# Performance work log

Measured on AMD Instinct MI355X. Metric: run time of the kernel, lower is better.

The kernel has to match this reference:

```python
import jax, jax.numpy as jnp
import numpy as np

N_NODES = 100000
N_EDGES = 1600000
IN_CH, HID_CH, OUT_CH = 128, 128, 64


def _spmm(row, col, val, x, n):
    # COO sparse @ dense: out[r] += val_e * x[col_e]
    gathered = val[:, None] * x[col]  # [E, d]
    return jax.ops.segment_sum(gathered, row, num_segments=n)


def setup_inputs() -> dict:
    key = jax.random.key(0)
    ks = jax.random.split(key, 8)
    x = jax.random.normal(ks[0], (N_NODES, IN_CH), dtype=jnp.float32)
    adj_row = jax.random.randint(ks[1], (N_EDGES,), 0, N_NODES)
    adj_col = jax.random.randint(ks[2], (N_EDGES,), 0, N_NODES)
    adj_val = jax.random.uniform(ks[3], (N_EDGES,), dtype=jnp.float32)
    w1 = jax.random.normal(ks[4], (IN_CH, HID_CH), dtype=jnp.float32) * (1.0 / np.sqrt(IN_CH))
    b1 = jax.random.normal(ks[5], (HID_CH,), dtype=jnp.float32) * 0.01
    w2 = jax.random.normal(ks[6], (HID_CH, OUT_CH), dtype=jnp.float32) * (1.0 / np.sqrt(HID_CH))
    b2 = jax.random.normal(ks[7], (OUT_CH,), dtype=jnp.float32) * 0.01
    return {"x": x, "adj_row": adj_row, "adj_col": adj_col, "adj_val": adj_val,
            "w1": w1, "b1": b1, "w2": w2, "b2": b2}


def reference(x, adj_row, adj_col, adj_val, w1, b1, w2, b2):
    n = x.shape[0]
    # layer 1: spmm -> linear -> relu
    h = _spmm(adj_row, adj_col, adj_val, x, n)
    h = jax.nn.relu(h @ w1 + b1)
    # layer 2: spmm -> linear
    h = _spmm(adj_row, adj_col, adj_val, h, n)
    return h @ w2 + b2
```

## Files before the change

kernel.cpp:

```cpp
#include <hip/hip_runtime.h>


typedef __bf16 v8bf __attribute__((ext_vector_type(8)));
typedef float  v4f  __attribute__((ext_vector_type(4)));

#define MAXB 800

__device__ __forceinline__ unsigned short f2bf(float f) {
    unsigned u = __float_as_uint(f);
    unsigned r = u + 0x7fffu + ((u >> 16) & 1u);
    return (unsigned short)(r >> 16);
}

__global__ __launch_bounds__(256) void hist_b(const int* __restrict__ arow,
                                              int* __restrict__ counts, int E, int B) {
    __shared__ int lh[MAXB];
    const int tid = threadIdx.x;
    for (int i = tid; i < B; i += 256) lh[i] = 0;
    __syncthreads();
    const int base = blockIdx.x * 4096;
#pragma unroll
    for (int j = 0; j < 16; ++j) {
        int i = base + j * 256 + tid;
        if (i < E) atomicAdd(&lh[arow[i] >> 7], 1);
    }
    __syncthreads();
    for (int i = tid; i < B; i += 256) {
        int c = lh[i];
        if (c) atomicAdd(&counts[i], c);
    }
}

__global__ __launch_bounds__(256) void scan_s(const int* __restrict__ counts,
                                              int* __restrict__ boff,
                                              int* __restrict__ gcursor,
                                              int* __restrict__ rowptr,
                                              int2* __restrict__ epkS,
                                              int B, int E, int N) {
    __shared__ int lds[256];
    const int t = threadIdx.x;
    const int b0 = t * 4;
    int v[4];
    int s = 0;
#pragma unroll
    for (int j = 0; j < 4; ++j) {
        v[j] = (b0 + j < B) ? counts[b0 + j] : 0;
        s += v[j];
    }
    lds[t] = s;
    __syncthreads();
    for (int off = 1; off < 256; off <<= 1) {
        int tmp = 0;
        if (t >= off) tmp = lds[t - off];
        __syncthreads();
        if (t >= off) lds[t] += tmp;
        __syncthreads();
    }
    int run = (t > 0) ? lds[t - 1] : 0;
#pragma unroll
    for (int j = 0; j < 4; ++j) {
        if (b0 + j < B) {
            boff[b0 + j] = run;
            gcursor[b0 + j] = run;
        }
        run += v[j];
    }
    if (t == 255) {
        boff[B] = E;
        rowptr[N] = E;
        epkS[E] = make_int2(0, 0);
        epkS[E + 1] = make_int2(0, 0);
        epkS[E + 2] = make_int2(0, 0);
    }
}

__global__ __launch_bounds__(256) void partition_k(const int* __restrict__ arow,
                                                   const int* __restrict__ acol,
                                                   const float* __restrict__ aval,
                                                   int* __restrict__ gcursor,
                                                   int2* __restrict__ epk, int E, int B) {
    __shared__ int2 ldata[4096];
    __shared__ int ldest[4096];
    __shared__ int lhist[MAXB];
    __shared__ int lscan[MAXB];
    __shared__ int ldelta[MAXB];
    __shared__ int lcur[MAXB];
    __shared__ int stmp[256];
    const int tid = threadIdx.x;
    const int base = blockIdx.x * 4096;
    const int cnt = min(4096, E - base);

    for (int i = tid; i < MAXB; i += 256) {
        lhist[i] = 0;
        lcur[i] = 0;
    }
    __syncthreads();

    int rr[16];
#pragma unroll
    for (int j = 0; j < 16; ++j) {
        int i = base + j * 256 + tid;
        rr[j] = (i < E) ? arow[i] : -1;
        if (rr[j] >= 0) atomicAdd(&lhist[rr[j] >> 7], 1);
    }
    __syncthreads();

    const int b0 = tid * 4;
    int v[4];
    int s = 0;
#pragma unroll
    for (int j = 0; j < 4; ++j) {
        v[j] = (b0 + j < MAXB) ? lhist[b0 + j] : 0;
        s += v[j];
    }
    stmp[tid] = s;
    __syncthreads();
    for (int off = 1; off < 256; off <<= 1) {
        int tmp = 0;
        if (tid >= off) tmp = stmp[tid - off];
        __syncthreads();
        if (tid >= off) stmp[tid] += tmp;
        __syncthreads();
    }
    int run = (tid > 0) ? stmp[tid - 1] : 0;
#pragma unroll
    for (int j = 0; j < 4; ++j) {
        if (b0 + j < MAXB) lscan[b0 + j] = run;
        run += v[j];
    }
    __syncthreads();

    for (int b = tid; b < B; b += 256) {
        int c = lhist[b];
        if (c) ldelta[b] = atomicAdd(&gcursor[b], c) - lscan[b];
    }
    __syncthreads();

#pragma unroll
    for (int j = 0; j < 16; ++j) {
        int i = base + j * 256 + tid;
        if (i < E) {
            int r = rr[j];
            int b = r >> 7;
            int lp = atomicAdd(&lcur[b], 1);
            int slot = lscan[b] + lp;
            int pk = acol[i] | ((r & 127) << 17);
            ldata[slot] = make_int2(pk, __float_as_int(aval[i]));
            ldest[slot] = ldelta[b] + slot;
        }
    }
    __syncthreads();

    for (int s2 = tid; s2 < cnt; s2 += 256) epk[ldest[s2]] = ldata[s2];
}

__global__ __launch_bounds__(256) void bucket_sort(const int* __restrict__ boff,
                                                   const int2* __restrict__ epk,
                                                   int2* __restrict__ epkS,
                                                   int* __restrict__ rowptr, int N) {
    __shared__ int2 sorted[4096];
    __shared__ int sc[128];
    __shared__ int lcur[128];
    const int tid = threadIdx.x;
    const int b = blockIdx.x;
    const int s = boff[b], e = boff[b + 1];
    const int cnt = min(e - s, 4096);
    if (tid < 128) sc[tid] = 0;
    __syncthreads();
    for (int i = s + tid; i < e; i += 256) {
        int rl = (epk[i].x >> 17) & 127;
        atomicAdd(&sc[rl], 1);
    }
    __syncthreads();
    int hv = (tid < 128) ? sc[tid] : 0;
    for (int off = 1; off < 128; off <<= 1) {
        int add = 0;
        if (tid < 128 && tid >= off) add = sc[tid - off];
        __syncthreads();
        if (tid < 128 && tid >= off) sc[tid] += add;
        __syncthreads();
    }
    if (tid < 128) {
        int ex = sc[tid] - hv;
        lcur[tid] = ex;
        int r = b * 128 + tid;
        if (r < N) rowptr[r] = s + ex;
    }
    __syncthreads();
    for (int i = s + tid; i < e; i += 256) {
        int2 p = epk[i];
        int rl = (p.x >> 17) & 127;
        int slot = atomicAdd(&lcur[rl], 1);
        if (slot < 4096) sorted[slot] = make_int2(p.x & 0x1FFFF, p.y);
    }
    __syncthreads();
    for (int i = tid; i < cnt; i += 256) epkS[s + i] = sorted[i];
}

__global__ void cast_transpose_w(const float* __restrict__ w, unsigned short* __restrict__ wT,
                                 int K, int NC) {
    int i = blockIdx.x * blockDim.x + threadIdx.x;
    if (i < K * NC) {
        int k = i / NC, n = i - k * NC;
        wT[n * K + k] = f2bf(w[i]);
    }
}

template <int NC, bool AF32>
__global__ __launch_bounds__(256) void gemm_mfma(const void* __restrict__ A,
                                                 const unsigned short* __restrict__ wT,
                                                 unsigned short* __restrict__ y, int M) {
    constexpr int KP = 136;
    constexpr int NT = NC / 16;
    __shared__ unsigned short wl[NC * KP];
    const int tid = threadIdx.x;
    for (int idx = tid; idx < NC * 16; idx += 256) {
        int n = idx >> 4, kc = idx & 15;
        *(uint4*)&wl[n * KP + kc * 8] = *(const uint4*)&wT[n * 128 + kc * 8];
    }
    __syncthreads();

    const int wave = tid >> 6;
    const int lane = tid & 63;
    const int m = lane & 15;
    const int q = lane >> 4;
    const int rowbase = blockIdx.x * 64 + wave * 16;
    const int rowc = min(rowbase + m, M - 1);

    v4f acc[NT] = {};
    union LU { uint4 qv; v8bf b; };

#pragma unroll
    for (int ks = 0; ks < 4; ++ks) {
        const int k0 = ks * 32 + q * 8;
        v8bf a;
        if (AF32) {
            const float* Ap = (const float*)A + (size_t)rowc * 128 + k0;
            float4 f0 = *(const float4*)Ap;
            float4 f1 = *(const float4*)(Ap + 4);
            union { unsigned short s[8]; v8bf b; } cv;
            cv.s[0] = f2bf(f0.x); cv.s[1] = f2bf(f0.y);
            cv.s[2] = f2bf(f0.z); cv.s[3] = f2bf(f0.w);
            cv.s[4] = f2bf(f1.x); cv.s[5] = f2bf(f1.y);
            cv.s[6] = f2bf(f1.z); cv.s[7] = f2bf(f1.w);
            a = cv.b;
        } else {
            LU lu;
            lu.qv = *(const uint4*)((const unsigned short*)A + (size_t)rowc * 128 + k0);
            a = lu.b;
        }
#pragma unroll
        for (int nt = 0; nt < NT; ++nt) {
            v8bf b = *(const v8bf*)&wl[(nt * 16 + m) * KP + k0];
            acc[nt] = __builtin_amdgcn_mfma_f32_16x16x32_bf16(a, b, acc[nt], 0, 0, 0);
        }
    }
#pragma unroll
    for (int nt = 0; nt < NT; ++nt) {
#pragma unroll
        for (int r = 0; r < 4; ++r) {
            int orow = rowbase + q * 4 + r;
            if (orow < M) y[(size_t)orow * NC + nt * 16 + m] = f2bf(acc[nt][r]);
        }
    }
}

template <int CH, bool RELU, bool OUT_BF16>
__global__ __launch_bounds__(256) void spmm_v2(const int* __restrict__ rowptr,
                                               const int2* __restrict__ ep,
                                               const unsigned short* __restrict__ yb,
                                               const float* __restrict__ bias,
                                               void* __restrict__ outp, int N) {
    const int row = (blockIdx.x * 256 + threadIdx.x) >> 6;
    const int lane = threadIdx.x & 63;
    if (row >= N) return;
    const int s = rowptr[row], e = rowptr[row + 1];
    float accx = 0.f, accy = 0.f;
    for (int j = s; j < e; j += 4) {
        int2 e0 = ep[j];
        int2 e1 = ep[j + 1];
        int2 e2 = ep[j + 2];
        int2 e3 = ep[j + 3];
        float v0 = __int_as_float(e0.y);
        float v1 = (j + 1 < e) ? __int_as_float(e1.y) : 0.f;
        float v2 = (j + 2 < e) ? __int_as_float(e2.y) : 0.f;
        float v3 = (j + 3 < e) ? __int_as_float(e3.y) : 0.f;
        if (CH == 128) {
            const unsigned* y32 = (const unsigned*)yb;
            unsigned u0 = y32[(size_t)e0.x * 64 + lane];
            unsigned u1 = y32[(size_t)e1.x * 64 + lane];
            unsigned u2 = y32[(size_t)e2.x * 64 + lane];
            unsigned u3 = y32[(size_t)e3.x * 64 + lane];
            accx += v0 * __uint_as_float(u0 << 16);
            accy += v0 * __uint_as_float(u0 & 0xffff0000u);
            accx += v1 * __uint_as_float(u1 << 16);
            accy += v1 * __uint_as_float(u1 & 0xffff0000u);
            accx += v2 * __uint_as_float(u2 << 16);
            accy += v2 * __uint_as_float(u2 & 0xffff0000u);
            accx += v3 * __uint_as_float(u3 << 16);
            accy += v3 * __uint_as_float(u3 & 0xffff0000u);
        } else {
            unsigned u0 = yb[(size_t)e0.x * 64 + lane];
            unsigned u1 = yb[(size_t)e1.x * 64 + lane];
            unsigned u2 = yb[(size_t)e2.x * 64 + lane];
            unsigned u3 = yb[(size_t)e3.x * 64 + lane];
            accx += v0 * __uint_as_float(u0 << 16);
            accx += v1 * __uint_as_float(u1 << 16);
            accx += v2 * __uint_as_float(u2 << 16);
            accx += v3 * __uint_as_float(u3 << 16);
        }
    }
    if (CH == 128) {
        float2 bv = ((const float2*)bias)[lane];
        accx += bv.x;
        accy += bv.y;
        if (RELU) { accx = fmaxf(accx, 0.f); accy = fmaxf(accy, 0.f); }
        if (OUT_BF16) {
            unsigned pk = ((unsigned)f2bf(accy) << 16) | f2bf(accx);
            ((unsigned*)outp)[(size_t)row * 64 + lane] = pk;
        } else {
            float2 o; o.x = accx; o.y = accy;
            ((float2*)outp)[(size_t)row * 64 + lane] = o;
        }
    } else {
        accx += bias[lane];
        if (RELU) accx = fmaxf(accx, 0.f);
        if (OUT_BF16) {
            ((unsigned short*)outp)[(size_t)row * 64 + lane] = f2bf(accx);
        } else {
            ((float*)outp)[(size_t)row * 64 + lane] = accx;
        }
    }
}

extern "C" void kernel_launch(void* const* d_in, const int* in_sizes, int n_in,
                              void* d_out, int out_size, void* d_ws, size_t ws_size,
                              hipStream_t stream) {
    const float* x    = (const float*)d_in[0];
    const int*   arow = (const int*)d_in[1];
    const int*   acol = (const int*)d_in[2];
    const float* aval = (const float*)d_in[3];
    const float* w1   = (const float*)d_in[4];
    const float* b1   = (const float*)d_in[5];
    const float* w2   = (const float*)d_in[6];
    const float* b2   = (const float*)d_in[7];
    float*       out  = (float*)d_out;

    const int N = in_sizes[0] / 128;
    const int E = in_sizes[1];
    const int B = (N + 127) >> 7;

    char* p = (char*)d_ws;
    auto alloc = [&](size_t bytes) {
        char* r = p;
        p += (bytes + 255) & ~(size_t)255;
        return r;
    };
    int*            counts  = (int*)alloc((size_t)MAXB * 4);
    int*            boff    = (int*)alloc((size_t)(MAXB + 1) * 4);
    int*            gcursor = (int*)alloc((size_t)MAXB * 4);
    int*            rowptr  = (int*)alloc((size_t)(N + 1) * 4);
    int2*           epkS    = (int2*)alloc((size_t)(E + 4) * 8);
    unsigned short* w1T     = (unsigned short*)alloc(128 * 128 * 2);
    unsigned short* w2T     = (unsigned short*)alloc(64 * 128 * 2);
    unsigned short* y1b     = (unsigned short*)alloc((size_t)N * 128 * 2);
    unsigned short* h1b     = (unsigned short*)alloc((size_t)N * 128 * 2);
    unsigned short* y2b     = (unsigned short*)alloc((size_t)N * 64 * 2);
    int2*           epk     = (int2*)h1b;

    hipMemsetAsync(counts, 0, (size_t)MAXB * 4, stream);
    const int pb = (E + 4095) / 4096;
    hist_b<<<pb, 256, 0, stream>>>(arow, counts, E, B);
    scan_s<<<1, 256, 0, stream>>>(counts, boff, gcursor, rowptr, epkS, B, E, N);
    partition_k<<<pb, 256, 0, stream>>>(arow, acol, aval, gcursor, epk, E, B);
    bucket_sort<<<B, 256, 0, stream>>>(boff, epk, epkS, rowptr, N);

    cast_transpose_w<<<(128 * 128 + 255) / 256, 256, 0, stream>>>(w1, w1T, 128, 128);
    cast_transpose_w<<<(128 * 64 + 255) / 256, 256, 0, stream>>>(w2, w2T, 128, 64);

    const int gemm_blocks = (N + 63) / 64;
    gemm_mfma<128, true><<<gemm_blocks, 256, 0, stream>>>(x, w1T, y1b, N);
    const int spmm_blocks = (N + 3) / 4;
    spmm_v2<128, true, true><<<spmm_blocks, 256, 0, stream>>>(rowptr, epkS, y1b, b1, h1b, N);

    gemm_mfma<64, false><<<gemm_blocks, 256, 0, stream>>>(h1b, w2T, y2b, N);
    spmm_v2<64, false, false><<<spmm_blocks, 256, 0, stream>>>(rowptr, epkS, y2b, b2, out, N);
}
```

Before: 324.7 us.

## Merge setup kernels, fuse bucket sort with first GEMM, prefetch edges in SpMM

Weight cast/transpose, counter zeroing and sentinel writes move into one prep kernel, which replaces a memset and two launches. The bucket sort and the first GEMM run as two block ranges of a single launch so they overlap. The SpMM kernels are specialised per width, unroll by 8 and prefetch the next batch of edge records into registers. The 64-wide SpMM splits edges across two half-waves, each reading 32-bit packed pairs, then combines them with a shuffle. Register pressure rises, and the prefetch can read past row ends, so the edge buffer padding grows to 32 entries.

```diff
diff --git a/kernel.cpp b/kernel.cpp
--- a/kernel.cpp
+++ b/kernel.cpp
@@ -10,6 +10,30 @@
     unsigned u = __float_as_uint(f);
     unsigned r = u + 0x7fffu + ((u >> 16) & 1u);
     return (unsigned short)(r >> 16);
+}
+
+__global__ __launch_bounds__(256) void prep_k(const float* __restrict__ w1,
+                                              const float* __restrict__ w2,
+                                              unsigned short* __restrict__ w1T,
+                                              unsigned short* __restrict__ w2T,
+                                              int* __restrict__ counts,
+                                              int* __restrict__ rowptr,
+                                              int2* __restrict__ epkS, int E, int N) {
+    int i = blockIdx.x * 256 + threadIdx.x;
+    if (i < 16384) {
+        int n = i >> 7, k = i & 127;
+        w1T[i] = f2bf(w1[k * 128 + n]);
+    } else if (i < 24576) {
+        int i2 = i - 16384;
+        int n = i2 >> 7, k = i2 & 127;
+        w2T[i2] = f2bf(w2[k * 64 + n]);
+    } else if (i < 24576 + MAXB) {
+        counts[i - 24576] = 0;
+    } else if (i < 24576 + MAXB + 32) {
+        epkS[E + (i - 24576 - MAXB)] = make_int2(0, 0);
+    } else if (i == 24576 + MAXB + 32) {
+        rowptr[N] = E;
+    }
 }
 
 __global__ __launch_bounds__(256) void hist_b(const int* __restrict__ arow,
@@ -33,10 +57,7 @@
 
 __global__ __launch_bounds__(256) void scan_s(const int* __restrict__ counts,
                                               int* __restrict__ boff,
-                                              int* __restrict__ gcursor,
-                                              int* __restrict__ rowptr,
-                                              int2* __restrict__ epkS,
-                                              int B, int E, int N) {
+                                              int* __restrict__ gcursor, int B, int E) {
     __shared__ int lds[256];
     const int t = threadIdx.x;
     const int b0 = t * 4;
@@ -65,13 +86,7 @@
         }
         run += v[j];
     }
-    if (t == 255) {
-        boff[B] = E;
-        rowptr[N] = E;
-        epkS[E] = make_int2(0, 0);
-        epkS[E + 1] = make_int2(0, 0);
-        epkS[E + 2] = make_int2(0, 0);
-    }
+    if (t == 255) boff[B] = E;
 }
 
 __global__ __launch_bounds__(256) void partition_k(const int* __restrict__ arow,
@@ -154,65 +169,14 @@
     for (int s2 = tid; s2 < cnt; s2 += 256) epk[ldest[s2]] = ldata[s2];
 }
 
-__global__ __launch_bounds__(256) void bucket_sort(const int* __restrict__ boff,
-                                                   const int2* __restrict__ epk,
-                                                   int2* __restrict__ epkS,
-                                                   int* __restrict__ rowptr, int N) {
-    __shared__ int2 sorted[4096];
-    __shared__ int sc[128];
-    __shared__ int lcur[128];
-    const int tid = threadIdx.x;
-    const int b = blockIdx.x;
-    const int s = boff[b], e = boff[b + 1];
-    const int cnt = min(e - s, 4096);
-    if (tid < 128) sc[tid] = 0;
-    __syncthreads();
-    for (int i = s + tid; i < e; i += 256) {
-        int rl = (epk[i].x >> 17) & 127;
-        atomicAdd(&sc[rl], 1);
-    }
-    __syncthreads();
-    int hv = (tid < 128) ? sc[tid] : 0;
-    for (int off = 1; off < 128; off <<= 1) {
-        int add = 0;
-        if (tid < 128 && tid >= off) add = sc[tid - off];
-        __syncthreads();
-        if (tid < 128 && tid >= off) sc[tid] += add;
-        __syncthreads();
-    }
-    if (tid < 128) {
-        int ex = sc[tid] - hv;
-        lcur[tid] = ex;
-        int r = b * 128 + tid;
-        if (r < N) rowptr[r] = s + ex;
-    }
-    __syncthreads();
-    for (int i = s + tid; i < e; i += 256) {
-        int2 p = epk[i];
-        int rl = (p.x >> 17) & 127;
-        int slot = atomicAdd(&lcur[rl], 1);
-        if (slot < 4096) sorted[slot] = make_int2(p.x & 0x1FFFF, p.y);
-    }
-    __syncthreads();
-    for (int i = tid; i < cnt; i += 256) epkS[s + i] = sorted[i];
-}
-
-__global__ void cast_transpose_w(const float* __restrict__ w, unsigned short* __restrict__ wT,
-                                 int K, int NC) {
-    int i = blockIdx.x * blockDim.x + threadIdx.x;
-    if (i < K * NC) {
-        int k = i / NC, n = i - k * NC;
-        wT[n * K + k] = f2bf(w[i]);
-    }
-}
-
 template <int NC, bool AF32>
-__global__ __launch_bounds__(256) void gemm_mfma(const void* __restrict__ A,
-                                                 const unsigned short* __restrict__ wT,
-                                                 unsigned short* __restrict__ y, int M) {
+__device__ __forceinline__ void gemm_body(const void* __restrict__ A,
+                                          const unsigned short* __restrict__ wT,
+                                          unsigned short* __restrict__ y, int M,
+                                          int bid, char* smem) {
     constexpr int KP = 136;
     constexpr int NT = NC / 16;
-    __shared__ unsigned short wl[NC * KP];
+    unsigned short* wl = (unsigned short*)smem;
     const int tid = threadIdx.x;
     for (int idx = tid; idx < NC * 16; idx += 256) {
         int n = idx >> 4, kc = idx & 15;
@@ -224,7 +188,7 @@
     const int lane = tid & 63;
     const int m = lane & 15;
     const int q = lane >> 4;
-    const int rowbase = blockIdx.x * 64 + wave * 16;
+    const int rowbase = bid * 64 + wave * 16;
     const int rowc = min(rowbase + m, M - 1);
 
     v4f acc[NT] = {};
@@ -265,71 +229,138 @@
     }
 }
 
-template <int CH, bool RELU, bool OUT_BF16>
-__global__ __launch_bounds__(256) void spmm_v2(const int* __restrict__ rowptr,
+__global__ __launch_bounds__(256) void sort_gemm1(const int* __restrict__ boff,
+                                                  const int2* __restrict__ epk,
+                                                  int2* __restrict__ epkS,
+                                                  int* __restrict__ rowptr, int N, int B,
+                                                  const float* __restrict__ x,
+                                                  const unsigned short* __restrict__ w1T,
+                                                  unsigned short* __restrict__ y1b) {
+    __shared__ __align__(16) char smem[34816];
+    const int tid = threadIdx.x;
+    if (blockIdx.x >= B) {
+        gemm_body<128, true>(x, w1T, y1b, N, blockIdx.x - B, smem);
+        return;
+    }
+    int2* sorted = (int2*)smem;
+    int*  sc     = (int*)(smem + 32768);
+    int*  lcur   = (int*)(smem + 32768 + 512);
+    const int b = blockIdx.x;
+    const int s = boff[b], e = boff[b + 1];
+    const int cnt = min(e - s, 4096);
+    if (tid < 128) sc[tid] = 0;
+    __syncthreads();
+    for (int i = s + tid; i < e; i += 256) {
+        int rl = (epk[i].x >> 17) & 127;
+        atomicAdd(&sc[rl], 1);
+    }
+    __syncthreads();
+    int hv = (tid < 128) ? sc[tid] : 0;
+    for (int off = 1; off < 128; off <<= 1) {
+        int add = 0;
+        if (tid < 128 && tid >= off) add = sc[tid - off];
+        __syncthreads();
+        if (tid < 128 && tid >= off) sc[tid] += add;
+        __syncthreads();
+    }
+    if (tid < 128) {
+        int ex = sc[tid] - hv;
+        lcur[tid] = ex;
+        int r = b * 128 + tid;
+        if (r < N) rowptr[r] = s + ex;
+    }
+    __syncthreads();
+    for (int i = s + tid; i < e; i += 256) {
+        int2 p = epk[i];
+        int rl = (p.x >> 17) & 127;
+        int slot = atomicAdd(&lcur[rl], 1);
+        if (slot < 4096) sorted[slot] = make_int2(p.x & 0x1FFFF, p.y);
+    }
+    __syncthreads();
+    for (int i = tid; i < cnt; i += 256) epkS[s + i] = sorted[i];
+}
+
+__global__ __launch_bounds__(256) void gemm2_k(const unsigned short* __restrict__ h1b,
+                                               const unsigned short* __restrict__ w2T,
+                                               unsigned short* __restrict__ y2b, int M) {
+    __shared__ __align__(16) char smem[64 * 136 * 2];
+    gemm_body<64, false>(h1b, w2T, y2b, M, blockIdx.x, smem);
+}
+
+__global__ __launch_bounds__(256) void spmm128(const int* __restrict__ rowptr,
                                                const int2* __restrict__ ep,
                                                const unsigned short* __restrict__ yb,
                                                const float* __restrict__ bias,
-                                               void* __restrict__ outp, int N) {
+                                               unsigned* __restrict__ outp, int N) {
     const int row = (blockIdx.x * 256 + threadIdx.x) >> 6;
     const int lane = threadIdx.x & 63;
     if (row >= N) return;
     const int s = rowptr[row], e = rowptr[row + 1];
+    const unsigned* y32 = (const unsigned*)yb;
     float accx = 0.f, accy = 0.f;
-    for (int j = s; j < e; j += 4) {
-        int2 e0 = ep[j];
-        int2 e1 = ep[j + 1];
-        int2 e2 = ep[j + 2];
-        int2 e3 = ep[j + 3];
-        float v0 = __int_as_float(e0.y);
-        float v1 = (j + 1 < e) ? __int_as_float(e1.y) : 0.f;
-        float v2 = (j + 2 < e) ? __int_as_float(e2.y) : 0.f;
-        float v3 = (j + 3 < e) ? __int_as_float(e3.y) : 0.f;
-        if (CH == 128) {
-            const unsigned* y32 = (const unsigned*)yb;
-            unsigned u0 = y32[(size_t)e0.x * 64 + lane];
-            unsigned u1 = y32[(size_t)e1.x * 64 + lane];
-            unsigned u2 = y32[(size_t)e2.x * 64 + lane];
-            unsigned u3 = y32[(size_t)e3.x * 64 + lane];
-            accx += v0 * __uint_as_float(u0 << 16);
-            accy += v0 * __uint_as_float(u0 & 0xffff0000u);
-            accx += v1 * __uint_as_float(u1 << 16);
-            accy += v1 * __uint_as_float(u1 & 0xffff0000u);
-            accx += v2 * __uint_as_float(u2 << 16);
-            accy += v2 * __uint_as_float(u2 & 0xffff0000u);
-            accx += v3 * __uint_as_float(u3 << 16);
-            accy += v3 * __uint_as_float(u3 & 0xffff0000u);
-        } else {
-            unsigned u0 = yb[(size_t)e0.x * 64 + lane];
-            unsigned u1 = yb[(size_t)e1.x * 64 + lane];
-            unsigned u2 = yb[(size_t)e2.x * 64 + lane];
-            unsigned u3 = yb[(size_t)e3.x * 64 + lane];
-            accx += v0 * __uint_as_float(u0 << 16);
-            accx += v1 * __uint_as_float(u1 << 16);
-            accx += v2 * __uint_as_float(u2 << 16);
-            accx += v3 * __uint_as_float(u3 << 16);
-        }
-    }
-    if (CH == 128) {
-        float2 bv = ((const float2*)bias)[lane];
-        accx += bv.x;
-        accy += bv.y;
-        if (RELU) { accx = fmaxf(accx, 0.f); accy = fmaxf(accy, 0.f); }
-        if (OUT_BF16) {
-            unsigned pk = ((unsigned)f2bf(accy) << 16) | f2bf(accx);
-            ((unsigned*)outp)[(size_t)row * 64 + lane] = pk;
-        } else {
-            float2 o; o.x = accx; o.y = accy;
-            ((float2*)outp)[(size_t)row * 64 + lane] = o;
-        }
-    } else {
-        accx += bias[lane];
-        if (RELU) accx = fmaxf(accx, 0.f);
-        if (OUT_BF16) {
-            ((unsigned short*)outp)[(size_t)row * 64 + lane] = f2bf(accx);
-        } else {
-            ((float*)outp)[(size_t)row * 64 + lane] = accx;
-        }
+    int2 cur[8];
+#pragma unroll
+    for (int k = 0; k < 8; ++k) cur[k] = ep[s + k];
+    for (int j = s; j < e; j += 8) {
+        int2 nxt[8];
+#pragma unroll
+        for (int k = 0; k < 8; ++k) nxt[k] = ep[j + 8 + k];
+#pragma unroll
+        for (int k = 0; k < 8; ++k) {
+            float v = (j + k < e) ? __int_as_float(cur[k].y) : 0.f;
+            unsigned u = y32[(size_t)cur[k].x * 64 + lane];
+            accx += v * __uint_as_float(u << 16);
+            accy += v * __uint_as_float(u & 0xffff0000u);
+        }
+#pragma unroll
+        for (int k = 0; k < 8; ++k) cur[k] = nxt[k];
+    }
+    float2 bv = ((const float2*)bias)[lane];
+    accx += bv.x;
+    accy += bv.y;
+    accx = fmaxf(accx, 0.f);
+    accy = fmaxf(accy, 0.f);
+    outp[(size_t)row * 64 + lane] = ((unsigned)f2bf(accy) << 16) | f2bf(accx);
+}
+
+__global__ __launch_bounds__(256) void spmm64(const int* __restrict__ rowptr,
+                                              const int2* __restrict__ ep,
+                                              const unsigned short* __restrict__ yb,
+                                              const float* __restrict__ bias,
+                                              float2* __restrict__ outp, int N) {
+    const int row = (blockIdx.x * 256 + threadIdx.x) >> 6;
+    const int lane = threadIdx.x & 63;
+    if (row >= N) return;
+    const int half = lane >> 5;
+    const int sl = lane & 31;
+    const int s = rowptr[row], e = rowptr[row + 1];
+    const unsigned* y32 = (const unsigned*)yb;
+    float accx = 0.f, accy = 0.f;
+    int2 cur[8];
+#pragma unroll
+    for (int k = 0; k < 8; ++k) cur[k] = ep[s + 2 * k + half];
+    for (int j = s; j < e; j += 16) {
+        int2 nxt[8];
+#pragma unroll
+        for (int k = 0; k < 8; ++k) nxt[k] = ep[j + 16 + 2 * k + half];
+#pragma unroll
+        for (int k = 0; k < 8; ++k) {
+            float v = (j + 2 * k + half < e) ? __int_as_float(cur[k].y) : 0.f;
+            unsigned u = y32[(size_t)cur[k].x * 32 + sl];
+            accx += v * __uint_as_float(u << 16);
+            accy += v * __uint_as_float(u & 0xffff0000u);
+        }
+#pragma unroll
+        for (int k = 0; k < 8; ++k) cur[k] = nxt[k];
+    }
+    accx += __shfl_xor(accx, 32, 64);
+    accy += __shfl_xor(accy, 32, 64);
+    if (sl == lane) {
+        float2 bv = ((const float2*)bias)[sl];
+        float2 o;
+        o.x = accx + bv.x;
+        o.y = accy + bv.y;
+        outp[(size_t)row * 32 + sl] = o;
     }
 }
 
@@ -360,7 +391,7 @@
     int*            boff    = (int*)alloc((size_t)(MAXB + 1) * 4);
     int*            gcursor = (int*)alloc((size_t)MAXB * 4);
     int*            rowptr  = (int*)alloc((size_t)(N + 1) * 4);
-    int2*           epkS    = (int2*)alloc((size_t)(E + 4) * 8);
+    int2*           epkS    = (int2*)alloc((size_t)(E + 32) * 8);
     unsigned short* w1T     = (unsigned short*)alloc(128 * 128 * 2);
     unsigned short* w2T     = (unsigned short*)alloc(64 * 128 * 2);
     unsigned short* y1b     = (unsigned short*)alloc((size_t)N * 128 * 2);
@@ -368,21 +399,18 @@
     unsigned short* y2b     = (unsigned short*)alloc((size_t)N * 64 * 2);
     int2*           epk     = (int2*)h1b;
 
-    hipMemsetAsync(counts, 0, (size_t)MAXB * 4, stream);
+    const int gemm_blocks = (N + 63) / 64;
     const int pb = (E + 4095) / 4096;
+
+    prep_k<<<(24576 + MAXB + 33 + 255) / 256, 256, 0, stream>>>(
+        w1, w2, w1T, w2T, counts, rowptr, epkS, E, N);
     hist_b<<<pb, 256, 0, stream>>>(arow, counts, E, B);
-    scan_s<<<1, 256, 0, stream>>>(counts, boff, gcursor, rowptr, epkS, B, E, N);
+    scan_s<<<1, 256, 0, stream>>>(counts, boff, gcursor, B, E);
     partition_k<<<pb, 256, 0, stream>>>(arow, acol, aval, gcursor, epk, E, B);
-    bucket_sort<<<B, 256, 0, stream>>>(boff, epk, epkS, rowptr, N);
-
-    cast_transpose_w<<<(128 * 128 + 255) / 256, 256, 0, stream>>>(w1, w1T, 128, 128);
-    cast_transpose_w<<<(128 * 64 + 255) / 256, 256, 0, stream>>>(w2, w2T, 128, 64);
-
-    const int gemm_blocks = (N + 63) / 64;
-    gemm_mfma<128, true><<<gemm_blocks, 256, 0, stream>>>(x, w1T, y1b, N);
+    sort_gemm1<<<B + gemm_blocks, 256, 0, stream>>>(boff, epk, epkS, rowptr, N, B,
+                                                    x, w1T, y1b);
     const int spmm_blocks = (N + 3) / 4;
-    spmm_v2<128, true, true><<<spmm_blocks, 256, 0, stream>>>(rowptr, epkS, y1b, b1, h1b, N);
-
-    gemm_mfma<64, false><<<gemm_blocks, 256, 0, stream>>>(h1b, w2T, y2b, N);
-    spmm_v2<64, false, false><<<spmm_blocks, 256, 0, stream>>>(rowptr, epkS, y2b, b2, out, N);
-}
+    spmm128<<<spmm_blocks, 256, 0, stream>>>(rowptr, epkS, y1b, b1, (unsigned*)h1b, N);
+    gemm2_k<<<gemm_blocks, 256, 0, stream>>>(h1b, w2T, y2b, N);
+    spmm64<<<spmm_blocks, 256, 0, stream>>>(rowptr, epkS, y2b, b2, (float2*)out, N);
+}
```

After: 321.4 us. Within noise of the previous version (-1.0%).
